# Kernel optimization log

Hardware: AMD Instinct MI355X
Metric: run time of the kernel (lower is better)

The kernel has to match this reference:

```python
import jax, jax.numpy as jnp
import numpy as np

B, C, H, W = 2, 64, 64, 64
DH = C // 2  # 32, projected channel dim

def setup_inputs() -> dict:
    key = jax.random.key(0)
    ks = jax.random.split(key, 9)
    x = jax.random.normal(ks[0], (B, C, H, W), dtype=jnp.float32)
    # 1x1 conv weights stored as [out_ch, in_ch] (kernel dims squeezed)
    w1 = jax.random.normal(ks[1], (DH, C), dtype=jnp.float32) * 0.05
    b1 = jax.random.normal(ks[2], (DH,), dtype=jnp.float32) * 0.05
    w2 = jax.random.normal(ks[3], (DH, C), dtype=jnp.float32) * 0.05
    b2 = jax.random.normal(ks[4], (DH,), dtype=jnp.float32) * 0.05
    w3 = jax.random.normal(ks[5], (DH, C), dtype=jnp.float32) * 0.05
    b3 = jax.random.normal(ks[6], (DH,), dtype=jnp.float32) * 0.05
    w4 = jax.random.normal(ks[7], (C, DH), dtype=jnp.float32) * 0.05
    b4 = jax.random.normal(ks[8], (C,), dtype=jnp.float32) * 0.05
    return {"x": x, "w1": w1, "b1": b1, "w2": w2, "b2": b2,
            "w3": w3, "b3": b3, "w4": w4, "b4": b4}

def _proj(x, w, b):
    # 1x1 conv then permute(0,2,3,1) then flatten(B,H,W) -> [N, DH]
    y = jnp.einsum('bchw,oc->bhwo', x, w) + b
    return y.reshape(-1, w.shape[0])

def reference(x, w1, b1, w2, b2, w3, b3, w4, b4):
    b_, c_, h_, w_ = x.shape
    q = _proj(x, w1, b1)   # [N, DH]
    k = _proj(x, w2, b2)   # [N, DH]
    v = _proj(x, w3, b3)   # [N, DH]
    att = q @ k.T                       # [N, N]
    att = jax.nn.softmax(att, axis=0)   # softmax over dim 0 (rows, per column)
    o = att @ v                         # [N, DH]
    o = o.reshape(b_, h_, w_, c_ // 2)
    # conv4 (1x1) on [B, DH, H, W] then residual
    y = jnp.einsum('bhwc,oc->bohw', o, w4) + b4[None, :, None, None]
    return y + x
```

## Files before the change

kernel.cpp:

```cpp
#include <hip/hip_runtime.h>
#include <hip/hip_bf16.h>

#define N_TOK   8192
#define DH      32
#define CCH     64
#define HWSZ    4096
#define LOG2E   1.4426950408889634f

typedef __attribute__((ext_vector_type(8))) short  bf16x8;
typedef __attribute__((ext_vector_type(4))) short  bf16x4;
typedef __attribute__((ext_vector_type(4))) float  f32x4;

static __device__ __forceinline__ short f2bf(float f) {
    __hip_bfloat16 h = __float2bfloat16(f);
    return __builtin_bit_cast(short, h);
}

static __device__ __forceinline__ bf16x8 load_frag8(const __hip_bfloat16* __restrict__ base,
                                                    int row0, int l) {
    const __hip_bfloat16* p = base + (size_t)(row0 + (l & 15)) * DH + ((l >> 4) << 3);
    return *reinterpret_cast<const bf16x8*>(p);
}

__global__ __launch_bounds__(256) void k_qk(
        const float* __restrict__ x,
        const float* __restrict__ w1, const float* __restrict__ b1,
        const float* __restrict__ w2, const float* __restrict__ b2,
        __hip_bfloat16* __restrict__ Qb, __hip_bfloat16* __restrict__ Kb) {
    __shared__ float4 w1s[16][32];
    __shared__ float4 w2s[16][32];
    int t = threadIdx.x;
    for (int i = t; i < 512; i += 256) {
        int cg = i >> 5, d = i & 31;
        w1s[cg][d] = *reinterpret_cast<const float4*>(w1 + d * CCH + cg * 4);
        w2s[cg][d] = *reinterpret_cast<const float4*>(w2 + d * CCH + cg * 4);
    }
    __syncthreads();
    int d = t & 31, nr = t >> 5;
    int n = blockIdx.x * 8 + nr;
    int b = n >> 12, hw = n & 4095;
    const float* xp = x + (size_t)b * (CCH * HWSZ) + hw;
    float aq = b1[d], ak = b2[d];
    #pragma unroll
    for (int cg = 0; cg < 16; ++cg) {
        float x0 = xp[(cg * 4 + 0) * HWSZ];
        float x1 = xp[(cg * 4 + 1) * HWSZ];
        float x2 = xp[(cg * 4 + 2) * HWSZ];
        float x3 = xp[(cg * 4 + 3) * HWSZ];
        float4 a = w1s[cg][d];
        aq = fmaf(a.x, x0, aq); aq = fmaf(a.y, x1, aq);
        aq = fmaf(a.z, x2, aq); aq = fmaf(a.w, x3, aq);
        float4 bb = w2s[cg][d];
        ak = fmaf(bb.x, x0, ak); ak = fmaf(bb.y, x1, ak);
        ak = fmaf(bb.z, x2, ak); ak = fmaf(bb.w, x3, ak);
    }
    Qb[(size_t)n * DH + d] = __float2bfloat16(aq * LOG2E);
    Kb[(size_t)n * DH + d] = __float2bfloat16(ak);
}

__global__ __launch_bounds__(512) void k_zv(
        const float* __restrict__ x,
        const float* __restrict__ w3, const float* __restrict__ b3,
        const __hip_bfloat16* __restrict__ Qb, const __hip_bfloat16* __restrict__ Kb,
        __hip_bfloat16* __restrict__ vpT) {
    __shared__ float w3s[2048];
    __shared__ float zsh[8][32];
    __shared__ float rzf[32];
    int t = threadIdx.x;
    {
        const float4* src = reinterpret_cast<const float4*>(w3);
        reinterpret_cast<float4*>(w3s)[t] = src[t];
    }
    int l = t & 63, w = t >> 6;
    int j0 = blockIdx.x * 32;
    bf16x8 ka0 = load_frag8(Kb, j0, l);
    bf16x8 ka1 = load_frag8(Kb, j0 + 16, l);
    float zac[8];
    #pragma unroll
    for (int k = 0; k < 8; ++k) zac[k] = 0.f;
    const f32x4 z4 = {0.f, 0.f, 0.f, 0.f};
    int i0 = w * 1024;
    #pragma unroll 2
    for (int i = i0; i < i0 + 1024; i += 16) {
        bf16x8 qf = load_frag8(Qb, i, l);
        f32x4 s0 = __builtin_amdgcn_mfma_f32_16x16x32_bf16(ka0, qf, z4, 0, 0, 0);
        f32x4 s1 = __builtin_amdgcn_mfma_f32_16x16x32_bf16(ka1, qf, z4, 0, 0, 0);
        #pragma unroll
        for (int r = 0; r < 4; ++r) {
            zac[r]     += __builtin_amdgcn_exp2f(s0[r]);
            zac[4 + r] += __builtin_amdgcn_exp2f(s1[r]);
        }
    }
    #pragma unroll
    for (int k = 0; k < 8; ++k) {
        float z = zac[k];
        z += __shfl_xor(z, 1); z += __shfl_xor(z, 2);
        z += __shfl_xor(z, 4); z += __shfl_xor(z, 8);
        zac[k] = z;
    }
    if ((l & 15) == 0) {
        int jr = (l >> 4) * 4;
        #pragma unroll
        for (int r = 0; r < 4; ++r) {
            zsh[w][jr + r]      = zac[r];
            zsh[w][16 + jr + r] = zac[4 + r];
        }
    }
    __syncthreads();
    if (t < 32) {
        float z = 0.f;
        #pragma unroll
        for (int w2 = 0; w2 < 8; ++w2) z += zsh[w2][t];
        rzf[t] = __builtin_amdgcn_rcpf(z);
    }
    __syncthreads();
    int jl = t & 31;
    int n  = j0 + jl;
    int b  = n >> 12, hw = n & 4095;
    const float* xp = x + (size_t)b * (CCH * HWSZ) + hw;
    int d0 = t >> 5;
    float a0 = b3[d0], a1 = b3[d0 + 16];
    #pragma unroll 8
    for (int c = 0; c < CCH; ++c) {
        float xv = xp[c * HWSZ];
        a0 = fmaf(w3s[d0 * CCH + c], xv, a0);
        a1 = fmaf(w3s[(d0 + 16) * CCH + c], xv, a1);
    }
    float rz = rzf[jl];
    vpT[(size_t)d0 * N_TOK + n]        = __float2bfloat16(a0 * rz);
    vpT[(size_t)(d0 + 16) * N_TOK + n] = __float2bfloat16(a1 * rz);
}

__global__ __launch_bounds__(512) void k_af(
        const __hip_bfloat16* __restrict__ Qb, const __hip_bfloat16* __restrict__ Kb,
        const __hip_bfloat16* __restrict__ vpT,
        const float* __restrict__ w4, const float* __restrict__ b4,
        const float* __restrict__ x, float* __restrict__ y) {
    __shared__ float osh[8][32][33];
    __shared__ float w4s[2048];
    __shared__ float o_red[32][33];
    int t = threadIdx.x;
    {
        const float4* src = reinterpret_cast<const float4*>(w4);
        reinterpret_cast<float4*>(w4s)[t] = src[t];
    }
    int l = t & 63, w = t >> 6;
    int i0 = blockIdx.x * 32;
    bf16x8 qb0 = load_frag8(Qb, i0, l);
    bf16x8 qb1 = load_frag8(Qb, i0 + 16, l);
    f32x4 a00 = {0.f,0.f,0.f,0.f}, a01 = a00, a10 = a00, a11 = a00;
    const f32x4 z4 = {0.f, 0.f, 0.f, 0.f};
    int lo16 = l & 15, hi4 = (l >> 4) << 2;
    const __hip_bfloat16* v0p = vpT + (size_t)lo16 * N_TOK;
    const __hip_bfloat16* v1p = vpT + (size_t)(lo16 + 16) * N_TOK;
    int jbase = w * 1024;
    #pragma unroll 2
    for (int jl = 0; jl < 1024; jl += 16) {
        int j = jbase + jl;
        bf16x8 kaf = load_frag8(Kb, j, l);
        bf16x4 va0 = *reinterpret_cast<const bf16x4*>(v0p + j + hi4);
        bf16x4 va1 = *reinterpret_cast<const bf16x4*>(v1p + j + hi4);
        f32x4 s0 = __builtin_amdgcn_mfma_f32_16x16x32_bf16(kaf, qb0, z4, 0, 0, 0);
        f32x4 s1 = __builtin_amdgcn_mfma_f32_16x16x32_bf16(kaf, qb1, z4, 0, 0, 0);
        bf16x4 e0, e1;
        #pragma unroll
        for (int r = 0; r < 4; ++r) {
            e0[r] = f2bf(__builtin_amdgcn_exp2f(s0[r]));
            e1[r] = f2bf(__builtin_amdgcn_exp2f(s1[r]));
        }
        a00 = __builtin_amdgcn_mfma_f32_16x16x16bf16_1k(va0, e0, a00, 0, 0, 0);
        a01 = __builtin_amdgcn_mfma_f32_16x16x16bf16_1k(va1, e0, a01, 0, 0, 0);
        a10 = __builtin_amdgcn_mfma_f32_16x16x16bf16_1k(va0, e1, a10, 0, 0, 0);
        a11 = __builtin_amdgcn_mfma_f32_16x16x16bf16_1k(va1, e1, a11, 0, 0, 0);
    }
    #pragma unroll
    for (int r = 0; r < 4; ++r) {
        osh[w][hi4 + r][lo16]           = a00[r];
        osh[w][16 + hi4 + r][lo16]      = a01[r];
        osh[w][hi4 + r][16 + lo16]      = a10[r];
        osh[w][16 + hi4 + r][16 + lo16] = a11[r];
    }
    __syncthreads();
    #pragma unroll
    for (int idx = t; idx < 1024; idx += 512) {
        int d = idx >> 5, i = idx & 31;
        float o = 0.f;
        #pragma unroll
        for (int w2 = 0; w2 < 8; ++w2) o += osh[w2][d][i];
        o_red[d][i] = o;
    }
    __syncthreads();
    int i = t & 31, c0 = t >> 5;
    int n = i0 + i, b = n >> 12, hw = n & 4095;
    #pragma unroll
    for (int c = c0; c < CCH; c += 16) {
        float acc = b4[c];
        #pragma unroll
        for (int d = 0; d < DH; ++d)
            acc = fmaf(w4s[c * DH + d], o_red[d][i], acc);
        size_t idx = (size_t)b * (CCH * HWSZ) + (size_t)c * HWSZ + hw;
        y[idx] = acc + x[idx];
    }
}

extern "C" void kernel_launch(void* const* d_in, const int* in_sizes, int n_in,
                              void* d_out, int out_size, void* d_ws, size_t ws_size,
                              hipStream_t stream) {
    const float* x  = (const float*)d_in[0];
    const float* w1 = (const float*)d_in[1];
    const float* b1 = (const float*)d_in[2];
    const float* w2 = (const float*)d_in[3];
    const float* b2 = (const float*)d_in[4];
    const float* w3 = (const float*)d_in[5];
    const float* b3 = (const float*)d_in[6];
    const float* w4 = (const float*)d_in[7];
    const float* b4 = (const float*)d_in[8];
    float* y = (float*)d_out;

    char* ws = (char*)d_ws;
    const size_t KB = 1024;
    __hip_bfloat16* Qb  = (__hip_bfloat16*)(ws);
    __hip_bfloat16* Kb  = (__hip_bfloat16*)(ws + 512 * KB);
    __hip_bfloat16* vpT = (__hip_bfloat16*)(ws + 1024 * KB);

    hipLaunchKernelGGL(k_qk, dim3(N_TOK / 8), dim3(256), 0, stream,
                       x, w1, b1, w2, b2, Qb, Kb);
    hipLaunchKernelGGL(k_zv, dim3(N_TOK / 32), dim3(512), 0, stream,
                       x, w3, b3, Qb, Kb, vpT);
    hipLaunchKernelGGL(k_af, dim3(N_TOK / 32), dim3(512), 0, stream,
                       Qb, Kb, vpT, w4, b4, x, y);
}
```

Before: 66.24 us.

## Use 1024-thread blocks in zv and af kernels to split the sequence across 16 waves

Doubles the block size of the normalizer/V-projection and attention kernels from 8 to 16 waves, so each wave scans half as many keys or queries. The cross-wave reduction in the attention kernel becomes two-phase: the first 8 waves write partials to shared memory and the last 8 add theirs in, and the epilogue work is redistributed over 1024 threads. The shared-memory row pad changes from 33 to 36. The goal is more waves in flight per CU to hide MFMA and exp latency with only 256 blocks, at the cost of an extra barrier, a single block per CU, and possible register pressure under the launch bound.

```diff
diff --git a/kernel.cpp b/kernel.cpp
--- a/kernel.cpp
+++ b/kernel.cpp
@@ -58,16 +58,16 @@
     Kb[(size_t)n * DH + d] = __float2bfloat16(ak);
 }
 
-__global__ __launch_bounds__(512) void k_zv(
+__global__ __launch_bounds__(1024, 1) void k_zv(
         const float* __restrict__ x,
         const float* __restrict__ w3, const float* __restrict__ b3,
         const __hip_bfloat16* __restrict__ Qb, const __hip_bfloat16* __restrict__ Kb,
         __hip_bfloat16* __restrict__ vpT) {
     __shared__ float w3s[2048];
-    __shared__ float zsh[8][32];
+    __shared__ float zsh[16][32];
     __shared__ float rzf[32];
     int t = threadIdx.x;
-    {
+    if (t < 512) {
         const float4* src = reinterpret_cast<const float4*>(w3);
         reinterpret_cast<float4*>(w3s)[t] = src[t];
     }
@@ -79,9 +79,9 @@
     #pragma unroll
     for (int k = 0; k < 8; ++k) zac[k] = 0.f;
     const f32x4 z4 = {0.f, 0.f, 0.f, 0.f};
-    int i0 = w * 1024;
+    int i0 = w * 512;
     #pragma unroll 2
-    for (int i = i0; i < i0 + 1024; i += 16) {
+    for (int i = i0; i < i0 + 512; i += 16) {
         bf16x8 qf = load_frag8(Qb, i, l);
         f32x4 s0 = __builtin_amdgcn_mfma_f32_16x16x32_bf16(ka0, qf, z4, 0, 0, 0);
         f32x4 s1 = __builtin_amdgcn_mfma_f32_16x16x32_bf16(ka1, qf, z4, 0, 0, 0);
@@ -110,37 +110,32 @@
     if (t < 32) {
         float z = 0.f;
         #pragma unroll
-        for (int w2 = 0; w2 < 8; ++w2) z += zsh[w2][t];
+        for (int w2 = 0; w2 < 16; ++w2) z += zsh[w2][t];
         rzf[t] = __builtin_amdgcn_rcpf(z);
     }
     __syncthreads();
     int jl = t & 31;
+    int d0 = t >> 5;
     int n  = j0 + jl;
     int b  = n >> 12, hw = n & 4095;
     const float* xp = x + (size_t)b * (CCH * HWSZ) + hw;
-    int d0 = t >> 5;
-    float a0 = b3[d0], a1 = b3[d0 + 16];
+    float a0 = b3[d0];
     #pragma unroll 8
-    for (int c = 0; c < CCH; ++c) {
-        float xv = xp[c * HWSZ];
-        a0 = fmaf(w3s[d0 * CCH + c], xv, a0);
-        a1 = fmaf(w3s[(d0 + 16) * CCH + c], xv, a1);
-    }
-    float rz = rzf[jl];
-    vpT[(size_t)d0 * N_TOK + n]        = __float2bfloat16(a0 * rz);
-    vpT[(size_t)(d0 + 16) * N_TOK + n] = __float2bfloat16(a1 * rz);
-}
-
-__global__ __launch_bounds__(512) void k_af(
+    for (int c = 0; c < CCH; ++c)
+        a0 = fmaf(w3s[d0 * CCH + c], xp[c * HWSZ], a0);
+    vpT[(size_t)d0 * N_TOK + n] = __float2bfloat16(a0 * rzf[jl]);
+}
+
+__global__ __launch_bounds__(1024, 1) void k_af(
         const __hip_bfloat16* __restrict__ Qb, const __hip_bfloat16* __restrict__ Kb,
         const __hip_bfloat16* __restrict__ vpT,
         const float* __restrict__ w4, const float* __restrict__ b4,
         const float* __restrict__ x, float* __restrict__ y) {
-    __shared__ float osh[8][32][33];
+    __shared__ float osh[8][32][36];
     __shared__ float w4s[2048];
-    __shared__ float o_red[32][33];
+    __shared__ float o_red[32][36];
     int t = threadIdx.x;
-    {
+    if (t < 512) {
         const float4* src = reinterpret_cast<const float4*>(w4);
         reinterpret_cast<float4*>(w4s)[t] = src[t];
     }
@@ -153,9 +148,9 @@
     int lo16 = l & 15, hi4 = (l >> 4) << 2;
     const __hip_bfloat16* v0p = vpT + (size_t)lo16 * N_TOK;
     const __hip_bfloat16* v1p = vpT + (size_t)(lo16 + 16) * N_TOK;
-    int jbase = w * 1024;
+    int jbase = w * 512;
     #pragma unroll 2
-    for (int jl = 0; jl < 1024; jl += 16) {
+    for (int jl = 0; jl < 512; jl += 16) {
         int j = jbase + jl;
         bf16x8 kaf = load_frag8(Kb, j, l);
         bf16x4 va0 = *reinterpret_cast<const bf16x4*>(v0p + j + hi4);
@@ -173,17 +168,29 @@
         a10 = __builtin_amdgcn_mfma_f32_16x16x16bf16_1k(va0, e1, a10, 0, 0, 0);
         a11 = __builtin_amdgcn_mfma_f32_16x16x16bf16_1k(va1, e1, a11, 0, 0, 0);
     }
-    #pragma unroll
-    for (int r = 0; r < 4; ++r) {
-        osh[w][hi4 + r][lo16]           = a00[r];
-        osh[w][16 + hi4 + r][lo16]      = a01[r];
-        osh[w][hi4 + r][16 + lo16]      = a10[r];
-        osh[w][16 + hi4 + r][16 + lo16] = a11[r];
-    }
-    __syncthreads();
-    #pragma unroll
-    for (int idx = t; idx < 1024; idx += 512) {
-        int d = idx >> 5, i = idx & 31;
+    if (w < 8) {
+        #pragma unroll
+        for (int r = 0; r < 4; ++r) {
+            osh[w][hi4 + r][lo16]           = a00[r];
+            osh[w][16 + hi4 + r][lo16]      = a01[r];
+            osh[w][hi4 + r][16 + lo16]      = a10[r];
+            osh[w][16 + hi4 + r][16 + lo16] = a11[r];
+        }
+    }
+    __syncthreads();
+    if (w >= 8) {
+        int ws = w - 8;
+        #pragma unroll
+        for (int r = 0; r < 4; ++r) {
+            osh[ws][hi4 + r][lo16]           += a00[r];
+            osh[ws][16 + hi4 + r][lo16]      += a01[r];
+            osh[ws][hi4 + r][16 + lo16]      += a10[r];
+            osh[ws][16 + hi4 + r][16 + lo16] += a11[r];
+        }
+    }
+    __syncthreads();
+    {
+        int d = t >> 5, i = t & 31;
         float o = 0.f;
         #pragma unroll
         for (int w2 = 0; w2 < 8; ++w2) o += osh[w2][d][i];
@@ -193,7 +200,7 @@
     int i = t & 31, c0 = t >> 5;
     int n = i0 + i, b = n >> 12, hw = n & 4095;
     #pragma unroll
-    for (int c = c0; c < CCH; c += 16) {
+    for (int c = c0; c < CCH; c += 32) {
         float acc = b4[c];
         #pragma unroll
         for (int d = 0; d < DH; ++d)
@@ -225,8 +232,8 @@
 
     hipLaunchKernelGGL(k_qk, dim3(N_TOK / 8), dim3(256), 0, stream,
                        x, w1, b1, w2, b2, Qb, Kb);
-    hipLaunchKernelGGL(k_zv, dim3(N_TOK / 32), dim3(512), 0, stream,
+    hipLaunchKernelGGL(k_zv, dim3(N_TOK / 32), dim3(1024), 0, stream,
                        x, w3, b3, Qb, Kb, vpT);
-    hipLaunchKernelGGL(k_af, dim3(N_TOK / 32), dim3(512), 0, stream,
+    hipLaunchKernelGGL(k_af, dim3(N_TOK / 32), dim3(1024), 0, stream,
                        Qb, Kb, vpT, w4, b4, x, y);
 }
```

Result: faster. 63.15 us (-4.7%).
